# Optimization experiments

Measured on AMD Instinct MI355X. Metric: run time of the kernel, lower is better.

## Reference

```python
import jax, jax.numpy as jnp
import numpy as np

H = 128          # hidden_dim
L = 3            # n_layers
G = 128          # num graphs in batch
BN_EPS = 1e-5


def setup_inputs() -> dict:
    key = jax.random.key(0)
    ks = jax.random.split(key, 16)
    N, E, ND, ED = 2048, 8192, 32, 16
    s = lambda k, shape, fan: jax.random.normal(k, shape, dtype=jnp.float32) / np.sqrt(fan)
    return {
        "x": jax.random.normal(ks[0], (N, ND), dtype=jnp.float32),
        "edge_index": jax.random.randint(ks[1], (2, E), 0, N),
        "edge_attr": jax.random.normal(ks[2], (E, ED), dtype=jnp.float32),
        "batch": jnp.sort(jax.random.randint(ks[3], (N,), 0, G)),
        "node_W": s(ks[4], (ND, H), ND),
        "node_b": jnp.zeros((H,), jnp.float32),
        "edge_W": s(ks[5], (L, ED, H * H), ED),
        "edge_b": jnp.zeros((L, H * H), jnp.float32),
        "root_W": s(ks[6], (L, H, H), H),
        "conv_bias": jnp.zeros((L, H), jnp.float32),
        "bn_gamma": jnp.ones((L, H), jnp.float32),
        "bn_beta": jnp.zeros((L, H), jnp.float32),
        "cls_W1": s(ks[7], (H, 64), H),
        "cls_b1": jnp.zeros((64,), jnp.float32),
        "cls_W2": s(ks[8], (64, 1), 64),
        "cls_b2": jnp.zeros((1,), jnp.float32),
    }


def _segment_mean(vals, ids, num_segments):
    ssum = jax.ops.segment_sum(vals, ids, num_segments=num_segments)
    cnt = jax.ops.segment_sum(jnp.ones((vals.shape[0],), vals.dtype), ids,
                              num_segments=num_segments)
    return ssum / jnp.maximum(cnt, 1.0)[:, None]


def reference(x, edge_index, edge_attr, batch, node_W, node_b, edge_W, edge_b,
              root_W, conv_bias, bn_gamma, bn_beta, cls_W1, cls_b1, cls_W2, cls_b2):
    N = x.shape[0]
    src, dst = edge_index[0], edge_index[1]
    h = x @ node_W + node_b                                   # [N, H]
    for l in range(L):
        # edge-conditioned weights: [E, H, H]
        W = (edge_attr @ edge_W[l] + edge_b[l]).reshape(-1, H, H)
        msg = jnp.einsum('ei,eio->eo', h[src], W)             # gather + per-edge matmul
        agg = _segment_mean(msg, dst, N)                      # scatter-mean
        x_new = h @ root_W[l] + agg + conv_bias[l]
        # BatchNorm (batch statistics, training-mode math)
        mu = jnp.mean(x_new, axis=0)
        var = jnp.var(x_new, axis=0)
        x_new = (x_new - mu) * jax.lax.rsqrt(var + BN_EPS) * bn_gamma[l] + bn_beta[l]
        x_new = jax.nn.relu(x_new)                            # dropout omitted (eval)
        h = h + x_new                                         # residual
    g = _segment_mean(h, batch, G)                            # global mean pool [G, H]
    out = jax.nn.relu(g @ cls_W1 + cls_b1) @ cls_W2 + cls_b2  # classifier
    return out.squeeze(-1)                                    # [G]
```

## Files before the change

kernel.cpp:

```cpp
#include <hip/hip_runtime.h>
#include <cstddef>
#include <cstdint>

#define H 128
#define EDIM 16
#define NLAYER 3
#define NSLICE 18
#define WCOLS (NSLICE * H)
#define PCOLS (EDIM * H)

typedef unsigned short ushort_t;
typedef unsigned int uint_t;
typedef __attribute__((ext_vector_type(8))) short bf16x8;
typedef __attribute__((ext_vector_type(4))) float f32x4;

__device__ __forceinline__ ushort_t f2bf(float f) {
    uint_t u = __builtin_bit_cast(uint_t, f);
    u += 0x7fffu + ((u >> 16) & 1u);
    return (ushort_t)(u >> 16);
}
__device__ __forceinline__ float bf_lo(uint_t u) {
    return __builtin_bit_cast(float, u << 16);
}
__device__ __forceinline__ float bf_hi(uint_t u) {
    return __builtin_bit_cast(float, u & 0xffff0000u);
}

__global__ __launch_bounds__(256) void setup_kernel(
    const int* __restrict__ dst, const int* __restrict__ batch,
    int* __restrict__ histD, float* __restrict__ cntG, int E, int N,
    const float* __restrict__ eW, const float* __restrict__ eb,
    const float* __restrict__ rW, ushort_t* __restrict__ Wt,
    const float* __restrict__ x, const float* __restrict__ nW,
    const float* __restrict__ nbias, float* __restrict__ h,
    ushort_t* __restrict__ hbf)
{
    __shared__ alignas(16) ushort_t tile[128][136];
    const int t = threadIdx.x;

    if (blockIdx.x < 32) {
        const int g = blockIdx.x * 256 + t;
        if (g < E) atomicAdd(&histD[dst[g]], 1);
        if (g < N) atomicAdd(&cntG[batch[g]], 1.f);
        return;
    }

    if (blockIdx.x < 86) {
        const int b = blockIdx.x - 32;
        const int l = b / NSLICE, s = b % NSLICE;
        const float* S = (s < 16) ? (eW + ((size_t)l * 16 + s) * (H * H))
                       : (s == 16 ? (eb + (size_t)l * H * H)
                                  : (rW + (size_t)l * H * H));
        const int k = t >> 1, o0 = (t & 1) * 64;
#pragma unroll
        for (int j = 0; j < 64; j += 4) {
            float4 v = *(const float4*)&S[(size_t)k * H + o0 + j];
            tile[k][o0 + j + 0] = f2bf(v.x);
            tile[k][o0 + j + 1] = f2bf(v.y);
            tile[k][o0 + j + 2] = f2bf(v.z);
            tile[k][o0 + j + 3] = f2bf(v.w);
        }
        __syncthreads();
        const int n = t >> 1, k0 = (t & 1) * 64;
        ushort_t* outp = Wt + ((size_t)l * WCOLS + s * H + n) * H + k0;
#pragma unroll 8
        for (int j = 0; j < 64; ++j) outp[j] = tile[k0 + j][n];
        return;
    }

    const int b2 = blockIdx.x - 86;
    const int bm = (b2 >> 1) * 64;
    const int bn = (b2 & 1) * 64;
    float (*As)[68] = (float (*)[68])(void*)tile;
    float (*Bs)[68] = ((float (*)[68])(void*)tile) + 16;

    const int tx = t & 15, ty = t >> 4;
    float acc[4][4];
#pragma unroll
    for (int i = 0; i < 4; ++i)
#pragma unroll
        for (int j = 0; j < 4; ++j) acc[i][j] = 0.f;

    const int ka = t & 15, ma = t >> 4;
    const int nb2 = t & 63, kb = t >> 6;

    for (int k0 = 0; k0 < 32; k0 += 16) {
#pragma unroll
        for (int r = 0; r < 4; ++r)
            As[ka][ma + 16 * r] = x[(size_t)(bm + ma + 16 * r) * 32 + k0 + ka];
#pragma unroll
        for (int r = 0; r < 4; ++r)
            Bs[kb + 4 * r][nb2] = nW[(size_t)(k0 + kb + 4 * r) * H + bn + nb2];
        __syncthreads();
#pragma unroll
        for (int kk = 0; kk < 16; ++kk) {
            const float4 a4 = *(const float4*)&As[kk][ty * 4];
            const float4 b4 = *(const float4*)&Bs[kk][tx * 4];
            const float a[4] = {a4.x, a4.y, a4.z, a4.w};
            const float b[4] = {b4.x, b4.y, b4.z, b4.w};
#pragma unroll
            for (int i = 0; i < 4; ++i)
#pragma unroll
                for (int j = 0; j < 4; ++j)
                    acc[i][j] = fmaf(a[i], b[j], acc[i][j]);
        }
        __syncthreads();
    }
#pragma unroll
    for (int i = 0; i < 4; ++i) {
        const int row = bm + ty * 4 + i;
        float4 v;
        v.x = acc[i][0] + nbias[bn + tx * 4 + 0];
        v.y = acc[i][1] + nbias[bn + tx * 4 + 1];
        v.z = acc[i][2] + nbias[bn + tx * 4 + 2];
        v.w = acc[i][3] + nbias[bn + tx * 4 + 3];
        *(float4*)&h[(size_t)row * H + bn + tx * 4] = v;
        ushort_t* o = &hbf[(size_t)row * H + bn + tx * 4];
        o[0] = f2bf(v.x); o[1] = f2bf(v.y); o[2] = f2bf(v.z); o[3] = f2bf(v.w);
    }
}

__global__ __launch_bounds__(256) void mfma_gemm(
    const ushort_t* __restrict__ hbf, const ushort_t* __restrict__ Wt,
    ushort_t* __restrict__ Pb, float* __restrict__ QR)
{
    __shared__ ushort_t As[64][136];
    __shared__ ushort_t Bs[128][136];
    const int tid = threadIdx.x;
    const int bx = blockIdx.x;
    const int n0 = bx * 128;
    const int v0 = blockIdx.y * 64;

    {
        const int row = tid >> 2, col0 = (tid & 3) * 32;
        const ushort_t* ga = hbf + (size_t)(v0 + row) * H + col0;
#pragma unroll
        for (int j = 0; j < 32; j += 8)
            *(uint4*)&As[row][col0 + j] = *(const uint4*)(ga + j);
    }
    {
        const int row = tid >> 1, col0 = (tid & 1) * 64;
        const ushort_t* gb = Wt + (size_t)(n0 + row) * H + col0;
#pragma unroll
        for (int j = 0; j < 64; j += 8)
            *(uint4*)&Bs[row][col0 + j] = *(const uint4*)(gb + j);
    }
    __syncthreads();

    const int wave = tid >> 6, lane = tid & 63;
    const int l15 = lane & 15, kg = lane >> 4;
    const int mrow = wave * 16 + l15;

    f32x4 acc0 = {0,0,0,0}, acc1 = {0,0,0,0}, acc2 = {0,0,0,0}, acc3 = {0,0,0,0};
    f32x4 acc4 = {0,0,0,0}, acc5 = {0,0,0,0}, acc6 = {0,0,0,0}, acc7 = {0,0,0,0};

#pragma unroll
    for (int s2 = 0; s2 < 4; ++s2) {
        const int k = s2 * 32 + kg * 8;
        bf16x8 a = *(const bf16x8*)&As[mrow][k];
        bf16x8 b0 = *(const bf16x8*)&Bs[0 * 16 + l15][k];
        bf16x8 b1 = *(const bf16x8*)&Bs[1 * 16 + l15][k];
        bf16x8 b2 = *(const bf16x8*)&Bs[2 * 16 + l15][k];
        bf16x8 b3 = *(const bf16x8*)&Bs[3 * 16 + l15][k];
        bf16x8 b4 = *(const bf16x8*)&Bs[4 * 16 + l15][k];
        bf16x8 b5 = *(const bf16x8*)&Bs[5 * 16 + l15][k];
        bf16x8 b6 = *(const bf16x8*)&Bs[6 * 16 + l15][k];
        bf16x8 b7 = *(const bf16x8*)&Bs[7 * 16 + l15][k];
        acc0 = __builtin_amdgcn_mfma_f32_16x16x32_bf16(a, b0, acc0, 0, 0, 0);
        acc1 = __builtin_amdgcn_mfma_f32_16x16x32_bf16(a, b1, acc1, 0, 0, 0);
        acc2 = __builtin_amdgcn_mfma_f32_16x16x32_bf16(a, b2, acc2, 0, 0, 0);
        acc3 = __builtin_amdgcn_mfma_f32_16x16x32_bf16(a, b3, acc3, 0, 0, 0);
        acc4 = __builtin_amdgcn_mfma_f32_16x16x32_bf16(a, b4, acc4, 0, 0, 0);
        acc5 = __builtin_amdgcn_mfma_f32_16x16x32_bf16(a, b5, acc5, 0, 0, 0);
        acc6 = __builtin_amdgcn_mfma_f32_16x16x32_bf16(a, b6, acc6, 0, 0, 0);
        acc7 = __builtin_amdgcn_mfma_f32_16x16x32_bf16(a, b7, acc7, 0, 0, 0);
    }

    const int row0 = v0 + wave * 16 + kg * 4;
    if (bx < 16) {
        ushort_t* op = Pb + (size_t)row0 * PCOLS
                     + (l15 >> 1) * 32 + (l15 & 1) + bx * 2;
#pragma unroll
        for (int r = 0; r < 4; ++r) {
            const size_t ro = (size_t)r * PCOLS;
            op[ro + 0 * 256] = f2bf(acc0[r]);
            op[ro + 1 * 256] = f2bf(acc1[r]);
            op[ro + 2 * 256] = f2bf(acc2[r]);
            op[ro + 3 * 256] = f2bf(acc3[r]);
            op[ro + 4 * 256] = f2bf(acc4[r]);
            op[ro + 5 * 256] = f2bf(acc5[r]);
            op[ro + 6 * 256] = f2bf(acc6[r]);
            op[ro + 7 * 256] = f2bf(acc7[r]);
        }
    } else {
        float* op = QR + (size_t)row0 * 256 + (bx - 16) * 128 + l15;
#pragma unroll
        for (int r = 0; r < 4; ++r) {
            const size_t ro = (size_t)r * 256;
            op[ro + 0 * 16] = acc0[r];
            op[ro + 1 * 16] = acc1[r];
            op[ro + 2 * 16] = acc2[r];
            op[ro + 3 * 16] = acc3[r];
            op[ro + 4 * 16] = acc4[r];
            op[ro + 5 * 16] = acc5[r];
            op[ro + 6 * 16] = acc6[r];
            op[ro + 7 * 16] = acc7[r];
        }
    }
}

__global__ __launch_bounds__(256) void edge_msg(
    const ushort_t* __restrict__ Pb, const float* __restrict__ QR,
    const float* __restrict__ ea, const int* __restrict__ srcArr,
    const int* __restrict__ dstArr, float* __restrict__ agg, int E)
{
    const int wave = threadIdx.x >> 6, lane = threadIdx.x & 63;
    const int e = blockIdx.x * 4 + wave;
    if (e >= E) return;
    const int s  = srcArr[e];
    const int dv = dstArr[e];
    const float* eap = ea + (size_t)e * EDIM;
    const float4 w0 = *(const float4*)(eap + 0);
    const float4 w1 = *(const float4*)(eap + 4);
    const float4 w2 = *(const float4*)(eap + 8);
    const float4 w3 = *(const float4*)(eap + 12);
    const float w[16] = {w0.x, w0.y, w0.z, w0.w, w1.x, w1.y, w1.z, w1.w,
                         w2.x, w2.y, w2.z, w2.w, w3.x, w3.y, w3.z, w3.w};
    const uint_t* prow = (const uint_t*)Pb + (size_t)s * (PCOLS / 2) + lane * 16;
    const uint4 pa = *(const uint4*)(prow + 0);
    const uint4 pb = *(const uint4*)(prow + 4);
    const uint4 pc = *(const uint4*)(prow + 8);
    const uint4 pd = *(const uint4*)(prow + 12);
    const uint_t pv[16] = {pa.x, pa.y, pa.z, pa.w, pb.x, pb.y, pb.z, pb.w,
                           pc.x, pc.y, pc.z, pc.w, pd.x, pd.y, pd.z, pd.w};
    const float2 q2 = *(const float2*)(QR + (size_t)s * 256 + 2 * lane);
    float m0 = q2.x, m1 = q2.y;
#pragma unroll
    for (int d = 0; d < EDIM; ++d) {
        m0 = fmaf(w[d], bf_lo(pv[d]), m0);
        m1 = fmaf(w[d], bf_hi(pv[d]), m1);
    }
    atomicAdd(&agg[(size_t)dv * H + 2 * lane], m0);
    atomicAdd(&agg[(size_t)dv * H + 2 * lane + 1], m1);
}

__global__ __launch_bounds__(256) void node_stats(
    float* __restrict__ agg, const float* __restrict__ QR,
    const int* __restrict__ histD, const float* __restrict__ conv_b,
    float* __restrict__ xnew, float* __restrict__ bnS, float* __restrict__ bnQ)
{
    __shared__ float sS[H];
    __shared__ float sQ[H];
    const int tid = threadIdx.x;
    const int c = tid & 127, half = tid >> 7;
    const int v0 = blockIdx.x * 8 + half * 4;
    const float cb = conv_b[c];
    float s = 0.f, q = 0.f;
#pragma unroll
    for (int j = 0; j < 4; ++j) {
        const int v = v0 + j;
        const int deg = histD[v];
        const float rc = 1.0f / (float)(deg > 0 ? deg : 1);
        const size_t ix = (size_t)v * H + c;
        const float val = agg[ix] * rc + QR[(size_t)v * 256 + H + c] + cb;
        xnew[ix] = val;
        agg[ix] = 0.f;
        s += val;
        q += val * val;
    }
    if (half == 0) { sS[c] = s; sQ[c] = q; }
    __syncthreads();
    if (half == 1) {
        atomicAdd(&bnS[c], sS[c] + s);
        atomicAdd(&bnQ[c], sQ[c] + q);
    }
}

__global__ __launch_bounds__(256) void bn_apply(
    float* __restrict__ h, ushort_t* __restrict__ hbf,
    const float* __restrict__ xnew,
    const float* __restrict__ bnS, const float* __restrict__ bnQ,
    const float* __restrict__ gamma, const float* __restrict__ beta,
    const int* __restrict__ batch, float* __restrict__ gsum, int N, int last)
{
    const int idx = blockIdx.x * 256 + threadIdx.x;
    const int c = idx & 127;
    const int v = idx >> 7;
    const float invN = 1.0f / (float)N;
    const float mu = bnS[c] * invN;
    const float var = bnQ[c] * invN - mu * mu;
    const float val = (xnew[idx] - mu) * rsqrtf(var + 1e-5f) * gamma[c] + beta[c];
    const float hn = h[idx] + fmaxf(val, 0.f);
    h[idx] = hn;
    hbf[idx] = f2bf(hn);
    if (last) atomicAdd(&gsum[batch[v] * H + c], hn);
}

__global__ void classifier_kernel(
    const float* __restrict__ gsum, const float* __restrict__ cntG,
    const float* __restrict__ W1, const float* __restrict__ b1,
    const float* __restrict__ W2, const float* __restrict__ b2,
    float* __restrict__ out)
{
    const int g = blockIdx.x;
    const int j = threadIdx.x;
    const float rc = 1.0f / fmaxf(cntG[g], 1.0f);
    float acc = b1[j];
#pragma unroll 8
    for (int i = 0; i < H; ++i)
        acc = fmaf(gsum[g * H + i] * rc, W1[i * 64 + j], acc);
    float pv = fmaxf(acc, 0.f) * W2[j];
#pragma unroll
    for (int off = 32; off > 0; off >>= 1)
        pv += __shfl_down(pv, off);
    if (j == 0) out[g] = pv + b2[0];
}

extern "C" void kernel_launch(void* const* d_in, const int* in_sizes, int n_in,
                              void* d_out, int out_size, void* d_ws, size_t ws_size,
                              hipStream_t stream)
{
    const float* x      = (const float*)d_in[0];
    const int*   eidx   = (const int*)  d_in[1];
    const float* eattr  = (const float*)d_in[2];
    const int*   batch  = (const int*)  d_in[3];
    const float* node_W = (const float*)d_in[4];
    const float* node_b = (const float*)d_in[5];
    const float* edge_W = (const float*)d_in[6];
    const float* edge_b = (const float*)d_in[7];
    const float* root_W = (const float*)d_in[8];
    const float* conv_b = (const float*)d_in[9];
    const float* gamma  = (const float*)d_in[10];
    const float* beta   = (const float*)d_in[11];
    const float* W1     = (const float*)d_in[12];
    const float* b1     = (const float*)d_in[13];
    const float* W2     = (const float*)d_in[14];
    const float* b2     = (const float*)d_in[15];
    float* out = (float*)d_out;

    const int N = in_sizes[0] / 32;
    const int E = in_sizes[1] / 2;
    const int G = out_size;

    int* histD  = (int*)d_ws;
    float* cntG = (float*)(histD + N);
    float* bnS  = cntG + G;
    float* bnQ  = bnS + NLAYER * H;
    float* gsum = bnQ + NLAYER * H;
    float* agg  = gsum + (size_t)G * H;
    float* h    = agg + (size_t)N * H;
    float* xnew = h + (size_t)N * H;
    ushort_t* hbf = (ushort_t*)(xnew + (size_t)N * H);
    ushort_t* Wt  = hbf + (size_t)N * H;
    ushort_t* Pb  = Wt + (size_t)NLAYER * WCOLS * H;
    float* QR   = (float*)(Pb + (size_t)N * PCOLS);

    const size_t zbytes = ((size_t)N + G + 2 * NLAYER * H
                         + (size_t)G * H + (size_t)N * H) * 4;
    hipMemsetAsync(d_ws, 0, zbytes, stream);

    const int* src = eidx;
    const int* dst = eidx + E;

    setup_kernel<<<150, 256, 0, stream>>>(
        dst, batch, histD, cntG, E, N, edge_W, edge_b, root_W, Wt,
        x, node_W, node_b, h, hbf);

    for (int l = 0; l < NLAYER; ++l) {
        mfma_gemm<<<dim3(NSLICE, N / 64), 256, 0, stream>>>(
            hbf, Wt + (size_t)l * WCOLS * H, Pb, QR);
        edge_msg<<<E / 4, 256, 0, stream>>>(
            Pb, QR, eattr, src, dst, agg, E);
        node_stats<<<N / 8, 256, 0, stream>>>(
            agg, QR, histD, conv_b + (size_t)l * H,
            xnew, bnS + l * H, bnQ + l * H);
        bn_apply<<<(N * H) / 256, 256, 0, stream>>>(
            h, hbf, xnew, bnS + l * H, bnQ + l * H,
            gamma + (size_t)l * H, beta + (size_t)l * H,
            batch, gsum, N, l == NLAYER - 1);
    }

    classifier_kernel<<<G, 64, 0, stream>>>(gsum, cntG, W1, b1, W2, b2, out);
}
```

Baseline: 245.6 us.

## Fuse BN stats and apply via grid barrier; change P layout for coalesced edge reads

Replaces the node_stats and bn_apply kernel pair with a single finish_kernel. It accumulates BatchNorm sums, spins on a global atomic counter as a grid-wide barrier, then applies normalisation, ReLU and the residual while the values are still in registers. This removes one launch per layer and the xnew round trip through memory. It also changes the Pb output layout so each lane in edge_msg reads one dword per edim slice with lane-contiguous addresses, instead of four 16-byte vectors. The barrier relies on all N/4 blocks being co-resident, which a host-side occupancy check guards, and it adds deadlock risk if that assumption fails.

```diff
diff --git a/kernel.cpp b/kernel.cpp
--- a/kernel.cpp
+++ b/kernel.cpp
@@ -178,19 +178,18 @@
 
     const int row0 = v0 + wave * 16 + kg * 4;
     if (bx < 16) {
-        ushort_t* op = Pb + (size_t)row0 * PCOLS
-                     + (l15 >> 1) * 32 + (l15 & 1) + bx * 2;
+        ushort_t* op = Pb + (size_t)row0 * PCOLS + bx * H + l15;
 #pragma unroll
         for (int r = 0; r < 4; ++r) {
             const size_t ro = (size_t)r * PCOLS;
-            op[ro + 0 * 256] = f2bf(acc0[r]);
-            op[ro + 1 * 256] = f2bf(acc1[r]);
-            op[ro + 2 * 256] = f2bf(acc2[r]);
-            op[ro + 3 * 256] = f2bf(acc3[r]);
-            op[ro + 4 * 256] = f2bf(acc4[r]);
-            op[ro + 5 * 256] = f2bf(acc5[r]);
-            op[ro + 6 * 256] = f2bf(acc6[r]);
-            op[ro + 7 * 256] = f2bf(acc7[r]);
+            op[ro + 0 * 16] = f2bf(acc0[r]);
+            op[ro + 1 * 16] = f2bf(acc1[r]);
+            op[ro + 2 * 16] = f2bf(acc2[r]);
+            op[ro + 3 * 16] = f2bf(acc3[r]);
+            op[ro + 4 * 16] = f2bf(acc4[r]);
+            op[ro + 5 * 16] = f2bf(acc5[r]);
+            op[ro + 6 * 16] = f2bf(acc6[r]);
+            op[ro + 7 * 16] = f2bf(acc7[r]);
         }
     } else {
         float* op = QR + (size_t)row0 * 256 + (bx - 16) * 128 + l15;
@@ -226,22 +225,81 @@
     const float4 w3 = *(const float4*)(eap + 12);
     const float w[16] = {w0.x, w0.y, w0.z, w0.w, w1.x, w1.y, w1.z, w1.w,
                          w2.x, w2.y, w2.z, w2.w, w3.x, w3.y, w3.z, w3.w};
-    const uint_t* prow = (const uint_t*)Pb + (size_t)s * (PCOLS / 2) + lane * 16;
-    const uint4 pa = *(const uint4*)(prow + 0);
-    const uint4 pb = *(const uint4*)(prow + 4);
-    const uint4 pc = *(const uint4*)(prow + 8);
-    const uint4 pd = *(const uint4*)(prow + 12);
-    const uint_t pv[16] = {pa.x, pa.y, pa.z, pa.w, pb.x, pb.y, pb.z, pb.w,
-                           pc.x, pc.y, pc.z, pc.w, pd.x, pd.y, pd.z, pd.w};
+    const uint_t* prow = (const uint_t*)Pb + (size_t)s * (PCOLS / 2) + lane;
     const float2 q2 = *(const float2*)(QR + (size_t)s * 256 + 2 * lane);
     float m0 = q2.x, m1 = q2.y;
 #pragma unroll
     for (int d = 0; d < EDIM; ++d) {
-        m0 = fmaf(w[d], bf_lo(pv[d]), m0);
-        m1 = fmaf(w[d], bf_hi(pv[d]), m1);
+        const uint_t u = prow[(size_t)d * 64];
+        m0 = fmaf(w[d], bf_lo(u), m0);
+        m1 = fmaf(w[d], bf_hi(u), m1);
     }
     atomicAdd(&agg[(size_t)dv * H + 2 * lane], m0);
     atomicAdd(&agg[(size_t)dv * H + 2 * lane + 1], m1);
+}
+
+__global__ __launch_bounds__(256, 2) void finish_kernel(
+    float* __restrict__ agg, const float* __restrict__ QR,
+    const int* __restrict__ histD, const float* __restrict__ conv_b,
+    const float* __restrict__ gamma, const float* __restrict__ beta,
+    float* __restrict__ h, ushort_t* __restrict__ hbf,
+    float* __restrict__ bnS, float* __restrict__ bnQ,
+    const int* __restrict__ batch, float* __restrict__ gsum,
+    int* __restrict__ cnt, int N, int last)
+{
+    __shared__ float sS[H];
+    __shared__ float sQ[H];
+    const int tid = threadIdx.x;
+    const int c = tid & 127, half = tid >> 7;
+    const int va = blockIdx.x * 4 + 2 * half;
+    const float cb = conv_b[c];
+    float vals[2];
+    float s = 0.f, q = 0.f;
+#pragma unroll
+    for (int j = 0; j < 2; ++j) {
+        const int v = va + j;
+        const int deg = histD[v];
+        const float rc = 1.0f / (float)(deg > 0 ? deg : 1);
+        const size_t ix = (size_t)v * H + c;
+        const float val = agg[ix] * rc + QR[(size_t)v * 256 + H + c] + cb;
+        vals[j] = val;
+        agg[ix] = 0.f;
+        s += val;
+        q += val * val;
+    }
+    if (half == 0) { sS[c] = s; sQ[c] = q; }
+    __syncthreads();
+    if (half == 1) {
+        atomicAdd(&bnS[c], sS[c] + s);
+        atomicAdd(&bnQ[c], sQ[c] + q);
+    }
+    __syncthreads();
+    if (tid == 0) {
+        __threadfence();
+        atomicAdd(cnt, 1);
+        while (__hip_atomic_load(cnt, __ATOMIC_ACQUIRE,
+                                 __HIP_MEMORY_SCOPE_AGENT) < (N >> 2)) {}
+    }
+    __syncthreads();
+
+    const float invN = 1.0f / (float)N;
+    const float S_ = __hip_atomic_load(&bnS[c], __ATOMIC_RELAXED,
+                                       __HIP_MEMORY_SCOPE_AGENT);
+    const float Q_ = __hip_atomic_load(&bnQ[c], __ATOMIC_RELAXED,
+                                       __HIP_MEMORY_SCOPE_AGENT);
+    const float mu = S_ * invN;
+    const float var = Q_ * invN - mu * mu;
+    const float sc = rsqrtf(var + 1e-5f) * gamma[c];
+    const float sh = beta[c] - mu * sc;
+#pragma unroll
+    for (int j = 0; j < 2; ++j) {
+        const int v = va + j;
+        const size_t ix = (size_t)v * H + c;
+        const float hn = h[ix] + fmaxf(vals[j] * sc + sh, 0.f);
+        h[ix] = hn;
+        if (!last) hbf[ix] = f2bf(hn);
+        else       atomicAdd(&gsum[batch[v] * H + c], hn);
+    }
 }
 
 __global__ __launch_bounds__(256) void node_stats(
@@ -346,7 +404,8 @@
     float* cntG = (float*)(histD + N);
     float* bnS  = cntG + G;
     float* bnQ  = bnS + NLAYER * H;
-    float* gsum = bnQ + NLAYER * H;
+    int* syncC  = (int*)(bnQ + NLAYER * H);
+    float* gsum = (float*)(syncC + 4);
     float* agg  = gsum + (size_t)G * H;
     float* h    = agg + (size_t)N * H;
     float* xnew = h + (size_t)N * H;
@@ -355,29 +414,49 @@
     ushort_t* Pb  = Wt + (size_t)NLAYER * WCOLS * H;
     float* QR   = (float*)(Pb + (size_t)N * PCOLS);
 
-    const size_t zbytes = ((size_t)N + G + 2 * NLAYER * H
+    const size_t zbytes = ((size_t)N + G + 2 * NLAYER * H + 4
                          + (size_t)G * H + (size_t)N * H) * 4;
     hipMemsetAsync(d_ws, 0, zbytes, stream);
 
     const int* src = eidx;
     const int* dst = eidx + E;
+
+    static int finish_ok = -1;
+    if (finish_ok < 0) {
+        int dev = 0, cus = 256, nb = 0;
+        (void)hipGetDevice(&dev);
+        if (hipDeviceGetAttribute(&cus, hipDeviceAttributeMultiprocessorCount,
+                                  dev) != hipSuccess || cus < 1) cus = 256;
+        if (hipOccupancyMaxActiveBlocksPerMultiprocessor(&nb, finish_kernel,
+                                  256, 0) != hipSuccess) nb = 0;
+        finish_ok = ((long long)nb * cus >= (N >> 2)) ? 1 : 0;
+    }
 
     setup_kernel<<<150, 256, 0, stream>>>(
         dst, batch, histD, cntG, E, N, edge_W, edge_b, root_W, Wt,
         x, node_W, node_b, h, hbf);
 
     for (int l = 0; l < NLAYER; ++l) {
+        const int last = (l == NLAYER - 1);
         mfma_gemm<<<dim3(NSLICE, N / 64), 256, 0, stream>>>(
             hbf, Wt + (size_t)l * WCOLS * H, Pb, QR);
         edge_msg<<<E / 4, 256, 0, stream>>>(
             Pb, QR, eattr, src, dst, agg, E);
-        node_stats<<<N / 8, 256, 0, stream>>>(
-            agg, QR, histD, conv_b + (size_t)l * H,
-            xnew, bnS + l * H, bnQ + l * H);
-        bn_apply<<<(N * H) / 256, 256, 0, stream>>>(
-            h, hbf, xnew, bnS + l * H, bnQ + l * H,
-            gamma + (size_t)l * H, beta + (size_t)l * H,
-            batch, gsum, N, l == NLAYER - 1);
+        if (finish_ok) {
+            finish_kernel<<<N / 4, 256, 0, stream>>>(
+                agg, QR, histD, conv_b + (size_t)l * H,
+                gamma + (size_t)l * H, beta + (size_t)l * H,
+                h, hbf, bnS + l * H, bnQ + l * H,
+                batch, gsum, syncC + l, N, last);
+        } else {
+            node_stats<<<N / 8, 256, 0, stream>>>(
+                agg, QR, histD, conv_b + (size_t)l * H,
+                xnew, bnS + l * H, bnQ + l * H);
+            bn_apply<<<(N * H) / 256, 256, 0, stream>>>(
+                h, hbf, xnew, bnS + l * H, bnQ + l * H,
+                gamma + (size_t)l * H, beta + (size_t)l * H,
+                batch, gsum, N, last);
+        }
     }
 
     classifier_kernel<<<G, 64, 0, stream>>>(gsum, cntG, W1, b1, W2, b2, out);
```

New measurement: 308.5 us. 1.26x slower.

## Change Pb layout to d-major for coalesced edge loads and vectorize bn_apply

Applied to the files above, without the earlier changes.

The GEMM now writes the bf16 P matrix so that each edge-dim slice is contiguous per node, rather than interleaved per lane. In edge_msg each lane then reads one 32-bit word per d, strided by 64 words, so the wave's loads coalesce instead of each lane pulling 64 contiguous bytes. bn_apply now handles four channels per thread with float4 loads and stores and a precomputed scale and shift, launching a quarter as many blocks. The GEMM epilogue store pattern changes, and edge_msg issues 16 separate loads instead of 4 wide ones.

```diff
diff --git a/kernel.cpp b/kernel.cpp
--- a/kernel.cpp
+++ b/kernel.cpp
@@ -178,19 +178,18 @@
 
     const int row0 = v0 + wave * 16 + kg * 4;
     if (bx < 16) {
-        ushort_t* op = Pb + (size_t)row0 * PCOLS
-                     + (l15 >> 1) * 32 + (l15 & 1) + bx * 2;
+        ushort_t* op = Pb + (size_t)row0 * PCOLS + bx * H + l15;
 #pragma unroll
         for (int r = 0; r < 4; ++r) {
             const size_t ro = (size_t)r * PCOLS;
-            op[ro + 0 * 256] = f2bf(acc0[r]);
-            op[ro + 1 * 256] = f2bf(acc1[r]);
-            op[ro + 2 * 256] = f2bf(acc2[r]);
-            op[ro + 3 * 256] = f2bf(acc3[r]);
-            op[ro + 4 * 256] = f2bf(acc4[r]);
-            op[ro + 5 * 256] = f2bf(acc5[r]);
-            op[ro + 6 * 256] = f2bf(acc6[r]);
-            op[ro + 7 * 256] = f2bf(acc7[r]);
+            op[ro + 0 * 16] = f2bf(acc0[r]);
+            op[ro + 1 * 16] = f2bf(acc1[r]);
+            op[ro + 2 * 16] = f2bf(acc2[r]);
+            op[ro + 3 * 16] = f2bf(acc3[r]);
+            op[ro + 4 * 16] = f2bf(acc4[r]);
+            op[ro + 5 * 16] = f2bf(acc5[r]);
+            op[ro + 6 * 16] = f2bf(acc6[r]);
+            op[ro + 7 * 16] = f2bf(acc7[r]);
         }
     } else {
         float* op = QR + (size_t)row0 * 256 + (bx - 16) * 128 + l15;
@@ -226,19 +225,14 @@
     const float4 w3 = *(const float4*)(eap + 12);
     const float w[16] = {w0.x, w0.y, w0.z, w0.w, w1.x, w1.y, w1.z, w1.w,
                          w2.x, w2.y, w2.z, w2.w, w3.x, w3.y, w3.z, w3.w};
-    const uint_t* prow = (const uint_t*)Pb + (size_t)s * (PCOLS / 2) + lane * 16;
-    const uint4 pa = *(const uint4*)(prow + 0);
-    const uint4 pb = *(const uint4*)(prow + 4);
-    const uint4 pc = *(const uint4*)(prow + 8);
-    const uint4 pd = *(const uint4*)(prow + 12);
-    const uint_t pv[16] = {pa.x, pa.y, pa.z, pa.w, pb.x, pb.y, pb.z, pb.w,
-                           pc.x, pc.y, pc.z, pc.w, pd.x, pd.y, pd.z, pd.w};
+    const uint_t* prow = (const uint_t*)Pb + (size_t)s * (PCOLS / 2) + lane;
     const float2 q2 = *(const float2*)(QR + (size_t)s * 256 + 2 * lane);
     float m0 = q2.x, m1 = q2.y;
 #pragma unroll
     for (int d = 0; d < EDIM; ++d) {
-        m0 = fmaf(w[d], bf_lo(pv[d]), m0);
-        m1 = fmaf(w[d], bf_hi(pv[d]), m1);
+        const uint_t u = prow[(size_t)d * 64];
+        m0 = fmaf(w[d], bf_lo(u), m0);
+        m1 = fmaf(w[d], bf_hi(u), m1);
     }
     atomicAdd(&agg[(size_t)dv * H + 2 * lane], m0);
     atomicAdd(&agg[(size_t)dv * H + 2 * lane + 1], m1);
@@ -283,17 +277,42 @@
     const float* __restrict__ gamma, const float* __restrict__ beta,
     const int* __restrict__ batch, float* __restrict__ gsum, int N, int last)
 {
-    const int idx = blockIdx.x * 256 + threadIdx.x;
-    const int c = idx & 127;
-    const int v = idx >> 7;
+    const int t4 = blockIdx.x * 256 + threadIdx.x;
+    const int c0 = (t4 & 31) * 4;
+    const int v = t4 >> 5;
+    const size_t ix = (size_t)t4 * 4;
     const float invN = 1.0f / (float)N;
-    const float mu = bnS[c] * invN;
-    const float var = bnQ[c] * invN - mu * mu;
-    const float val = (xnew[idx] - mu) * rsqrtf(var + 1e-5f) * gamma[c] + beta[c];
-    const float hn = h[idx] + fmaxf(val, 0.f);
-    h[idx] = hn;
-    hbf[idx] = f2bf(hn);
-    if (last) atomicAdd(&gsum[batch[v] * H + c], hn);
+    const float4 S4 = *(const float4*)&bnS[c0];
+    const float4 Q4 = *(const float4*)&bnQ[c0];
+    const float4 g4 = *(const float4*)&gamma[c0];
+    const float4 b4 = *(const float4*)&beta[c0];
+    float4 mu, sc, sh;
+    mu.x = S4.x * invN; mu.y = S4.y * invN; mu.z = S4.z * invN; mu.w = S4.w * invN;
+    sc.x = rsqrtf(Q4.x * invN - mu.x * mu.x + 1e-5f) * g4.x;
+    sc.y = rsqrtf(Q4.y * invN - mu.y * mu.y + 1e-5f) * g4.y;
+    sc.z = rsqrtf(Q4.z * invN - mu.z * mu.z + 1e-5f) * g4.z;
+    sc.w = rsqrtf(Q4.w * invN - mu.w * mu.w + 1e-5f) * g4.w;
+    sh.x = b4.x - mu.x * sc.x; sh.y = b4.y - mu.y * sc.y;
+    sh.z = b4.z - mu.z * sc.z; sh.w = b4.w - mu.w * sc.w;
+    const float4 xv = *(const float4*)&xnew[ix];
+    const float4 hv = *(const float4*)&h[ix];
+    float4 hn;
+    hn.x = hv.x + fmaxf(xv.x * sc.x + sh.x, 0.f);
+    hn.y = hv.y + fmaxf(xv.y * sc.y + sh.y, 0.f);
+    hn.z = hv.z + fmaxf(xv.z * sc.z + sh.z, 0.f);
+    hn.w = hv.w + fmaxf(xv.w * sc.w + sh.w, 0.f);
+    *(float4*)&h[ix] = hn;
+    uint2 u;
+    u.x = (uint_t)f2bf(hn.x) | ((uint_t)f2bf(hn.y) << 16);
+    u.y = (uint_t)f2bf(hn.z) | ((uint_t)f2bf(hn.w) << 16);
+    *(uint2*)&hbf[ix] = u;
+    if (last) {
+        float* gp = &gsum[batch[v] * H + c0];
+        atomicAdd(gp + 0, hn.x);
+        atomicAdd(gp + 1, hn.y);
+        atomicAdd(gp + 2, hn.z);
+        atomicAdd(gp + 3, hn.w);
+    }
 }
 
 __global__ void classifier_kernel(
@@ -374,7 +393,7 @@
         node_stats<<<N / 8, 256, 0, stream>>>(
             agg, QR, histD, conv_b + (size_t)l * H,
             xnew, bnS + l * H, bnQ + l * H);
-        bn_apply<<<(N * H) / 256, 256, 0, stream>>>(
+        bn_apply<<<(N * H) / 1024, 256, 0, stream>>>(
             h, hbf, xnew, bnS + l * H, bnQ + l * H,
             gamma + (size_t)l * H, beta + (size_t)l * H,
             batch, gsum, N, l == NLAYER - 1);
```

Measured after the change: 203.8 us. 1.2x faster.
